# Optimization experiments

Measured on AMD Instinct MI355X. Metric: run time of the kernel, lower is better.

## Reference

```python
import jax, jax.numpy as jnp
import numpy as np

COMP_TOKEN_ID = 7
R = 8
LORA_ALPHA = 16
SCALING = LORA_ALPHA / R  # 2.0


def setup_inputs() -> dict:
    key = jax.random.key(0)
    k1, k2, k3, k4, k5, k6 = jax.random.split(key, 6)
    B, S, D_IN, D_OUT = 4, 4096, 4096, 4096
    x = jax.random.normal(k1, (B, S, D_IN), dtype=jnp.float32)
    ids = jax.random.randint(k2, (B, S), 0, 64, dtype=jnp.int64)
    W = jax.random.normal(k3, (D_OUT, D_IN), dtype=jnp.float32) * (1.0 / np.sqrt(D_IN))
    b = jax.random.normal(k4, (D_OUT,), dtype=jnp.float32) * 0.02
    lora_A = jax.random.normal(k5, (R, D_IN), dtype=jnp.float32) * (1.0 / np.sqrt(D_IN))
    lora_B = jax.random.normal(k6, (D_OUT, R), dtype=jnp.float32) * 0.02
    return {"x": x, "ids": ids, "W": W, "b": b, "lora_A": lora_A, "lora_B": lora_B}


def reference(x, ids, W, b, lora_A, lora_B):
    # Base frozen linear: [B,S,d_in] @ [d_in,d_out] -> [B,S,d_out]
    base = jnp.einsum('bsi,oi->bso', x, W) + b
    # LoRA path (dropout is identity in eval mode): x @ A.T @ B.T * scaling
    lora = jnp.einsum('bsr,or->bso', jnp.einsum('bsi,ri->bsr', x, lora_A), lora_B) * SCALING
    # Per-token gate: only compression tokens get the LoRA update
    mask = (ids == COMP_TOKEN_ID).astype(x.dtype)[..., None]  # [B,S,1]
    return base + lora * mask
```

## Files before the change

kernel.cpp:

```cpp
#include <hip/hip_runtime.h>
#include <hip/hip_bf16.h>
#include <stdint.h>


typedef __attribute__((ext_vector_type(8))) __bf16 bf16x8;
typedef __attribute__((ext_vector_type(4))) float f32x4;

#define M_DIM 16384
#define K_DIM 4096
#define N_DIM 4096
#define BM 256
#define BN 256
#define BK 64
#define NT2 (K_DIM / BK)

__global__ void cvt_f32_bf16(const float* __restrict__ in, __hip_bfloat16* __restrict__ out, int n8) {
    int i = blockIdx.x * blockDim.x + threadIdx.x;
    int stride = gridDim.x * blockDim.x;
    for (; i < n8; i += stride) {
        const float4* p = (const float4*)(in + (size_t)i * 8);
        float4 v0 = p[0], v1 = p[1];
        bf16x8 o;
        o[0] = (__bf16)v0.x; o[1] = (__bf16)v0.y; o[2] = (__bf16)v0.z; o[3] = (__bf16)v0.w;
        o[4] = (__bf16)v1.x; o[5] = (__bf16)v1.y; o[6] = (__bf16)v1.z; o[7] = (__bf16)v1.w;
        *(bf16x8*)((__hip_bfloat16*)out + (size_t)i * 8) = o;
    }
}

__global__ void compute_xa(const __hip_bfloat16* __restrict__ Xb,
                           const int* __restrict__ ids,
                           const float* __restrict__ A,
                           float* __restrict__ xa) {
    int t = threadIdx.x;
    int r = t & 63;
    int kq = t >> 6;
    int row = blockIdx.x * 64 + r;
    const __hip_bfloat16* xrow = Xb + (size_t)row * K_DIM + kq * 1024;
    float acc[8] = {0.f, 0.f, 0.f, 0.f, 0.f, 0.f, 0.f, 0.f};
    for (int i = 0; i < 128; i++) {
        bf16x8 xv = *(const bf16x8*)(xrow + i * 8);
        int kk = kq * 1024 + i * 8;
#pragma unroll
        for (int rr = 0; rr < 8; rr++) {
            const float* ap = A + rr * K_DIM + kk;
            float4 a0 = *(const float4*)ap;
            float4 a1 = *(const float4*)(ap + 4);
            acc[rr] += (float)xv[0] * a0.x + (float)xv[1] * a0.y + (float)xv[2] * a0.z + (float)xv[3] * a0.w
                     + (float)xv[4] * a1.x + (float)xv[5] * a1.y + (float)xv[6] * a1.z + (float)xv[7] * a1.w;
        }
    }
    __shared__ float red[4][64][8];
#pragma unroll
    for (int rr = 0; rr < 8; rr++) red[kq][r][rr] = acc[rr];
    __syncthreads();
    if (t < 64) {
        int rowg = blockIdx.x * 64 + t;
        float gate = (ids[rowg] == 7) ? 2.0f : 0.0f;
#pragma unroll
        for (int rr = 0; rr < 8; rr++) {
            float s = (red[0][t][rr] + red[1][t][rr]) + (red[2][t][rr] + red[3][t][rr]);
            xa[(size_t)rowg * 8 + rr] = s * gate;
        }
    }
}

__device__ __forceinline__ void gload_lds16(const void* g, void* l) {
    __builtin_amdgcn_global_load_lds(
        (const __attribute__((address_space(1))) unsigned int*)g,
        (__attribute__((address_space(3))) unsigned int*)l, 16, 0, 0);
}

#define LGKM0()  asm volatile("s_waitcnt lgkmcnt(0)" ::: "memory")
#define VMC4()   asm volatile("s_waitcnt vmcnt(4)" ::: "memory")
#define VMC0()   asm volatile("s_waitcnt vmcnt(0)" ::: "memory")
#define BAR()    __builtin_amdgcn_s_barrier()
#define PRIO(p)  __builtin_amdgcn_s_setprio(p)

__global__ __launch_bounds__(512, 1) void gemm_bias_lora(
    const __hip_bfloat16* __restrict__ Xb,
    const __hip_bfloat16* __restrict__ Wb,
    const float* __restrict__ bias,
    const float* __restrict__ xa,
    const float* __restrict__ loraB,
    float* __restrict__ out) {
    __shared__ char smem[2 * 65536];

    int tid = threadIdx.x;
    int bid = blockIdx.x;
    int swz = (bid & 7) * 128 + (bid >> 3);
    int n_tile = swz & 15;
    int m_tile = swz >> 4;
    int m_base = m_tile * BM, n_base = n_tile * BN;
    int wave = tid >> 6, lane = tid & 63;
    int wr = wave >> 2, wc = wave & 3;
    int l15 = lane & 15, lhi = lane >> 4;
    int l8 = lane >> 3;
    int cx = ((lane & 7) ^ l8) * 16;
    int pswz0 = ((lhi)     ^ (l15 & 7)) * 16;
    int pswz1 = ((4 + lhi) ^ (l15 & 7)) * 16;

    f32x4 acc[8][4] = {};

    const char* Abase = (const char*)(Xb + (size_t)m_base * K_DIM);
    const char* Bbase = (const char*)(Wb + (size_t)n_base * K_DIM);

    auto stage_A = [&](int kt, int mq, int buf) {
        char* ub = smem + buf * 65536 + mq * 16384;
#pragma unroll
        for (int j = 0; j < 2; j++) {
            int rg = wave * 2 + j;
            int rl = rg * 8 + l8;
            int g = (rl < 64) ? (mq * 64 + rl) : (128 + mq * 64 + (rl - 64));
            gload_lds16(Abase + (size_t)g * (K_DIM * 2) + (size_t)kt * 128 + cx,
                        ub + rg * 1024 + lane * 16);
        }
    };
    auto stage_B = [&](int kt, int h, int buf) {
        char* ub = smem + buf * 65536 + 32768 + h * 16384;
#pragma unroll
        for (int j = 0; j < 2; j++) {
            int rg = wave * 2 + j;
            int row = h * 128 + rg * 8 + l8;
            gload_lds16(Bbase + (size_t)row * (K_DIM * 2) + (size_t)kt * 128 + cx,
                        ub + rg * 1024 + lane * 16);
        }
    };

    stage_A(0, 0, 0); stage_B(0, 0, 0); stage_B(0, 1, 0); stage_A(0, 1, 0);
    stage_A(1, 0, 1);
    VMC0();
    BAR();

    for (int t = 0; t < NT2; t++) {
        int cur = t & 1, nb = cur ^ 1;
        const char* aU0 = smem + cur * 65536 + (wr * 64 + l15) * 128;
        const char* aU1 = aU0 + 16384;
        const char* bRb = smem + cur * 65536 + 32768 + (wc * 64 + l15) * 128;
        bf16x8 af[4], bfr[4];

#pragma unroll
        for (int mi = 0; mi < 4; mi++) af[mi] = *(const bf16x8*)(aU0 + mi * 2048 + pswz0);
#pragma unroll
        for (int ni = 0; ni < 4; ni++) bfr[ni] = *(const bf16x8*)(bRb + ni * 2048 + pswz0);
        if (t + 1 < NT2) stage_B(t + 1, 0, nb);
        BAR();
        LGKM0();
        PRIO(1);
#pragma unroll
        for (int mi = 0; mi < 4; mi++)
#pragma unroll
            for (int ni = 0; ni < 4; ni++)
                acc[mi][ni] = __builtin_amdgcn_mfma_f32_16x16x32_bf16(af[mi], bfr[ni], acc[mi][ni], 0, 0, 0);
        PRIO(0);
        VMC4();
        BAR();

#pragma unroll
        for (int mi = 0; mi < 4; mi++) af[mi] = *(const bf16x8*)(aU1 + mi * 2048 + pswz0);
        if (t + 1 < NT2) stage_B(t + 1, 1, nb);
        BAR();
        LGKM0();
        PRIO(1);
#pragma unroll
        for (int mi = 0; mi < 4; mi++)
#pragma unroll
            for (int ni = 0; ni < 4; ni++)
                acc[4 + mi][ni] = __builtin_amdgcn_mfma_f32_16x16x32_bf16(af[mi], bfr[ni], acc[4 + mi][ni], 0, 0, 0);
        PRIO(0);
        BAR();

#pragma unroll
        for (int mi = 0; mi < 4; mi++) af[mi] = *(const bf16x8*)(aU0 + mi * 2048 + pswz1);
#pragma unroll
        for (int ni = 0; ni < 4; ni++) bfr[ni] = *(const bf16x8*)(bRb + ni * 2048 + pswz1);
        if (t + 1 < NT2) stage_A(t + 1, 1, nb);
        BAR();
        LGKM0();
        PRIO(1);
#pragma unroll
        for (int mi = 0; mi < 4; mi++)
#pragma unroll
            for (int ni = 0; ni < 4; ni++)
                acc[mi][ni] = __builtin_amdgcn_mfma_f32_16x16x32_bf16(af[mi], bfr[ni], acc[mi][ni], 0, 0, 0);
        PRIO(0);
        BAR();

#pragma unroll
        for (int mi = 0; mi < 4; mi++) af[mi] = *(const bf16x8*)(aU1 + mi * 2048 + pswz1);
        if (t + 2 < NT2) stage_A(t + 2, 0, cur);
        BAR();
        LGKM0();
        PRIO(1);
#pragma unroll
        for (int mi = 0; mi < 4; mi++)
#pragma unroll
            for (int ni = 0; ni < 4; ni++)
                acc[4 + mi][ni] = __builtin_amdgcn_mfma_f32_16x16x32_bf16(af[mi], bfr[ni], acc[4 + mi][ni], 0, 0, 0);
        PRIO(0);
        if (t < NT2 - 2) { VMC4(); } else { VMC0(); }
        BAR();
    }

    int wrow = m_base + wr * 128;
    int wcol = n_base + wc * 64;
    float bv[4];
    float4 lb0[4], lb1[4];
#pragma unroll
    for (int ni = 0; ni < 4; ni++) {
        int n = wcol + ni * 16 + l15;
        bv[ni] = bias[n];
        lb0[ni] = *(const float4*)(loraB + (size_t)n * 8);
        lb1[ni] = *(const float4*)(loraB + (size_t)n * 8 + 4);
    }
#pragma unroll
    for (int mi = 0; mi < 8; mi++) {
#pragma unroll
        for (int r = 0; r < 4; r++) {
            int m = wrow + mi * 16 + lhi * 4 + r;
            float4 xa0 = *(const float4*)(xa + (size_t)m * 8);
            float4 xa1 = *(const float4*)(xa + (size_t)m * 8 + 4);
#pragma unroll
            for (int ni = 0; ni < 4; ni++) {
                int n = wcol + ni * 16 + l15;
                float lora = xa0.x * lb0[ni].x + xa0.y * lb0[ni].y + xa0.z * lb0[ni].z + xa0.w * lb0[ni].w
                           + xa1.x * lb1[ni].x + xa1.y * lb1[ni].y + xa1.z * lb1[ni].z + xa1.w * lb1[ni].w;
                out[(size_t)m * N_DIM + n] = acc[mi][ni][r] + bv[ni] + lora;
            }
        }
    }
}

__global__ void fallback_kernel(const float* __restrict__ x, const int* __restrict__ ids,
                                const float* __restrict__ W, const float* __restrict__ b,
                                const float* __restrict__ A, const float* __restrict__ B8,
                                float* __restrict__ out) {
    __shared__ float xs[K_DIM];
    __shared__ float xa_s[8];
    int row = blockIdx.y;
    int t = threadIdx.x;
    const float* xr = x + (size_t)row * K_DIM;
    for (int k = t; k < K_DIM; k += 256) xs[k] = xr[k];
    __syncthreads();
    if (t < 8) {
        float s = 0.f;
        for (int k = 0; k < K_DIM; k++) s += xs[k] * A[t * K_DIM + k];
        xa_s[t] = (ids[row] == 7) ? s * 2.0f : 0.0f;
    }
    __syncthreads();
    int col = blockIdx.x * 256 + t;
    const float* wr = W + (size_t)col * K_DIM;
    float acc = 0.f;
    for (int k = 0; k < K_DIM; k++) acc += xs[k] * wr[k];
    float lora = 0.f;
#pragma unroll
    for (int rr = 0; rr < 8; rr++) lora += xa_s[rr] * B8[col * 8 + rr];
    out[(size_t)row * N_DIM + col] = acc + b[col] + lora;
}

extern "C" void kernel_launch(void* const* d_in, const int* in_sizes, int n_in,
                              void* d_out, int out_size, void* d_ws, size_t ws_size,
                              hipStream_t stream) {
    const float* x   = (const float*)d_in[0];
    const int*   ids = (const int*)d_in[1];
    const float* W   = (const float*)d_in[2];
    const float* b   = (const float*)d_in[3];
    const float* lA  = (const float*)d_in[4];
    const float* lB  = (const float*)d_in[5];
    float* out = (float*)d_out;

    size_t wb_bytes = (size_t)N_DIM * K_DIM * 2;
    size_t xb_bytes = (size_t)M_DIM * K_DIM * 2;
    size_t xa_bytes = (size_t)M_DIM * 8 * 4;

    if (ws_size >= wb_bytes + xb_bytes + xa_bytes) {
        __hip_bfloat16* Wb = (__hip_bfloat16*)d_ws;
        __hip_bfloat16* Xb = (__hip_bfloat16*)((char*)d_ws + wb_bytes);
        float* xa = (float*)((char*)d_ws + wb_bytes + xb_bytes);

        cvt_f32_bf16<<<1024, 256, 0, stream>>>(W, Wb, (int)((size_t)N_DIM * K_DIM / 8));
        cvt_f32_bf16<<<2048, 256, 0, stream>>>(x, Xb, (int)((size_t)M_DIM * K_DIM / 8));
        compute_xa<<<M_DIM / 64, 256, 0, stream>>>(Xb, ids, lA, xa);
        gemm_bias_lora<<<(M_DIM / BM) * (N_DIM / BN), 512, 0, stream>>>(Xb, Wb, b, xa, lB, out);
    } else {
        fallback_kernel<<<dim3(N_DIM / 256, M_DIM), 256, 0, stream>>>(x, ids, W, b, lA, lB, out);
    }
}
```

Baseline: 672.1 us.

## Restructure GEMM main loop with double register fragments and fewer barriers

Reworks the K-loop of the bf16 MFMA GEMM so A/B fragments are held in two register sets (af0/af1, bf0/bf1). LDS reads for the next MFMA group are issued before the current group runs, with partial lgkmcnt waits and sched_barrier fences. Barriers per iteration drop from eight to two, and the global-to-LDS staging is regrouped so vmcnt waits can leave stores pending. The aim is to overlap LDS latency with matrix math and cut synchronisation stalls. In exchange it uses more registers and relies on hand-counted waitcnt values being correct.

```diff
diff --git a/kernel.cpp b/kernel.cpp
--- a/kernel.cpp
+++ b/kernel.cpp
@@ -70,9 +70,9 @@
         (__attribute__((address_space(3))) unsigned int*)l, 16, 0, 0);
 }
 
-#define LGKM0()  asm volatile("s_waitcnt lgkmcnt(0)" ::: "memory")
-#define VMC4()   asm volatile("s_waitcnt vmcnt(4)" ::: "memory")
-#define VMC0()   asm volatile("s_waitcnt vmcnt(0)" ::: "memory")
+#define LGKMW(n) asm volatile("s_waitcnt lgkmcnt(" #n ")" ::: "memory")
+#define VMCW(n)  asm volatile("s_waitcnt vmcnt(" #n ")" ::: "memory")
+#define SB0()    __builtin_amdgcn_sched_barrier(0)
 #define BAR()    __builtin_amdgcn_s_barrier()
 #define PRIO(p)  __builtin_amdgcn_s_setprio(p)
 
@@ -128,76 +128,69 @@
 
     stage_A(0, 0, 0); stage_B(0, 0, 0); stage_B(0, 1, 0); stage_A(0, 1, 0);
     stage_A(1, 0, 1);
-    VMC0();
+    VMCW(2);
     BAR();
+
+    bf16x8 af0[4], af1[4], bf0[4], bf1[4];
 
     for (int t = 0; t < NT2; t++) {
         int cur = t & 1, nb = cur ^ 1;
         const char* aU0 = smem + cur * 65536 + (wr * 64 + l15) * 128;
         const char* aU1 = aU0 + 16384;
         const char* bRb = smem + cur * 65536 + 32768 + (wc * 64 + l15) * 128;
-        bf16x8 af[4], bfr[4];
-
-#pragma unroll
-        for (int mi = 0; mi < 4; mi++) af[mi] = *(const bf16x8*)(aU0 + mi * 2048 + pswz0);
-#pragma unroll
-        for (int ni = 0; ni < 4; ni++) bfr[ni] = *(const bf16x8*)(bRb + ni * 2048 + pswz0);
+
+#pragma unroll
+        for (int mi = 0; mi < 4; mi++) af0[mi] = *(const bf16x8*)(aU0 + mi * 2048 + pswz0);
+#pragma unroll
+        for (int ni = 0; ni < 4; ni++) bf0[ni] = *(const bf16x8*)(bRb + ni * 2048 + pswz0);
+#pragma unroll
+        for (int mi = 0; mi < 4; mi++) af1[mi] = *(const bf16x8*)(aU1 + mi * 2048 + pswz0);
         if (t + 1 < NT2) stage_B(t + 1, 0, nb);
+        LGKMW(4); SB0();
+        PRIO(1);
+#pragma unroll
+        for (int mi = 0; mi < 4; mi++)
+#pragma unroll
+            for (int ni = 0; ni < 4; ni++)
+                acc[mi][ni] = __builtin_amdgcn_mfma_f32_16x16x32_bf16(af0[mi], bf0[ni], acc[mi][ni], 0, 0, 0);
+        PRIO(0);
+
+#pragma unroll
+        for (int mi = 0; mi < 4; mi++) af0[mi] = *(const bf16x8*)(aU0 + mi * 2048 + pswz1);
+#pragma unroll
+        for (int ni = 0; ni < 4; ni++) bf1[ni] = *(const bf16x8*)(bRb + ni * 2048 + pswz1);
+        if (t + 1 < NT2) { stage_B(t + 1, 1, nb); stage_A(t + 1, 1, nb); }
+        LGKMW(8); SB0();
+        PRIO(1);
+#pragma unroll
+        for (int mi = 0; mi < 4; mi++)
+#pragma unroll
+            for (int ni = 0; ni < 4; ni++)
+                acc[4 + mi][ni] = __builtin_amdgcn_mfma_f32_16x16x32_bf16(af1[mi], bf0[ni], acc[4 + mi][ni], 0, 0, 0);
+        PRIO(0);
+
+#pragma unroll
+        for (int mi = 0; mi < 4; mi++) af1[mi] = *(const bf16x8*)(aU1 + mi * 2048 + pswz1);
+        LGKMW(4); SB0();
+        PRIO(1);
+#pragma unroll
+        for (int mi = 0; mi < 4; mi++)
+#pragma unroll
+            for (int ni = 0; ni < 4; ni++)
+                acc[mi][ni] = __builtin_amdgcn_mfma_f32_16x16x32_bf16(af0[mi], bf1[ni], acc[mi][ni], 0, 0, 0);
+        PRIO(0);
         BAR();
-        LGKM0();
-        PRIO(1);
-#pragma unroll
-        for (int mi = 0; mi < 4; mi++)
-#pragma unroll
-            for (int ni = 0; ni < 4; ni++)
-                acc[mi][ni] = __builtin_amdgcn_mfma_f32_16x16x32_bf16(af[mi], bfr[ni], acc[mi][ni], 0, 0, 0);
-        PRIO(0);
-        VMC4();
-        BAR();
-
-#pragma unroll
-        for (int mi = 0; mi < 4; mi++) af[mi] = *(const bf16x8*)(aU1 + mi * 2048 + pswz0);
-        if (t + 1 < NT2) stage_B(t + 1, 1, nb);
-        BAR();
-        LGKM0();
-        PRIO(1);
-#pragma unroll
-        for (int mi = 0; mi < 4; mi++)
-#pragma unroll
-            for (int ni = 0; ni < 4; ni++)
-                acc[4 + mi][ni] = __builtin_amdgcn_mfma_f32_16x16x32_bf16(af[mi], bfr[ni], acc[4 + mi][ni], 0, 0, 0);
-        PRIO(0);
-        BAR();
-
-#pragma unroll
-        for (int mi = 0; mi < 4; mi++) af[mi] = *(const bf16x8*)(aU0 + mi * 2048 + pswz1);
-#pragma unroll
-        for (int ni = 0; ni < 4; ni++) bfr[ni] = *(const bf16x8*)(bRb + ni * 2048 + pswz1);
-        if (t + 1 < NT2) stage_A(t + 1, 1, nb);
-        BAR();
-        LGKM0();
-        PRIO(1);
-#pragma unroll
-        for (int mi = 0; mi < 4; mi++)
-#pragma unroll
-            for (int ni = 0; ni < 4; ni++)
-                acc[mi][ni] = __builtin_amdgcn_mfma_f32_16x16x32_bf16(af[mi], bfr[ni], acc[mi][ni], 0, 0, 0);
-        PRIO(0);
-        BAR();
-
-#pragma unroll
-        for (int mi = 0; mi < 4; mi++) af[mi] = *(const bf16x8*)(aU1 + mi * 2048 + pswz1);
+
         if (t + 2 < NT2) stage_A(t + 2, 0, cur);
-        BAR();
-        LGKM0();
-        PRIO(1);
-#pragma unroll
-        for (int mi = 0; mi < 4; mi++)
-#pragma unroll
-            for (int ni = 0; ni < 4; ni++)
-                acc[4 + mi][ni] = __builtin_amdgcn_mfma_f32_16x16x32_bf16(af[mi], bfr[ni], acc[4 + mi][ni], 0, 0, 0);
-        PRIO(0);
-        if (t < NT2 - 2) { VMC4(); } else { VMC0(); }
+        LGKMW(0); SB0();
+        PRIO(1);
+#pragma unroll
+        for (int mi = 0; mi < 4; mi++)
+#pragma unroll
+            for (int ni = 0; ni < 4; ni++)
+                acc[4 + mi][ni] = __builtin_amdgcn_mfma_f32_16x16x32_bf16(af1[mi], bf1[ni], acc[4 + mi][ni], 0, 0, 0);
+        PRIO(0);
+        if (t < NT2 - 2) { VMCW(2); } else { VMCW(0); }
         BAR();
     }
 
```

Measured after the change: 654.2 us. 2.7% less time.
